# Kernel tuning notes

Hardware: AMD Instinct MI355X
Metric: run time of the kernel (lower is better)

## Reference

```python
import jax, jax.numpy as jnp
import numpy as np


def _ln(x):
    m = jnp.mean(x, axis=-1, keepdims=True)
    v = jnp.var(x, axis=-1, keepdims=True)
    return (x - m) * jax.lax.rsqrt(v + 1e-5)


def _forward(ql, cl, plm, ada_g_w, ada_g_b, ada_b_w, wq, bq, wk, wv, z_ln_g, z_ln_b, wz, wg, wo, sg_w, sg_b, ada2_g_w, ada2_g_b, ada2_b_w, ff1, ff2, ff3, sg2_w, sg2_b, n_queries, n_keys):
    B, N, C = ql.shape
    NB, _, D = wq.shape
    H = wz.shape[-1]
    DH = D // H
    # AF3-style 32x128 blocked local attention bias (additive mask), as in source
    centers = jnp.arange(N // n_queries + 1, dtype=jnp.float32) * n_queries + (n_queries / 2 - 0.5)
    pos = jnp.arange(N, dtype=jnp.float32)
    row = jnp.abs(pos[:, None] - centers[None, :]) < n_queries / 2   # [N, n_centers]
    col = jnp.abs(pos[:, None] - centers[None, :]) < n_keys / 2     # [N, n_centers]
    BIG = jnp.float32(1e10)
    blm = jnp.sum((row[:, None, :] & col[None, :, :]).astype(jnp.float32), axis=-1) * BIG - BIG  # [N, N], 0 or -1e10
    s_ln = _ln(cl)  # conditioning signal, shared LN across blocks
    a = ql
    for i in range(NB):  # DiffusionTransformer (AF3 Alg 23)
        # AttentionPairBias with AdaLN conditioning (Alg 24/26)
        x = jax.nn.sigmoid(s_ln @ ada_g_w[i] + ada_g_b[i]) * _ln(a) + s_ln @ ada_b_w[i]
        q = (x @ wq[i] + bq[i]).reshape(B, N, H, DH)
        k = (x @ wk[i]).reshape(B, N, H, DH)
        v = (x @ wv[i]).reshape(B, N, H, DH)
        zb = jnp.einsum('bqkc,ch->bhqk', _ln(plm) * z_ln_g[i] + z_ln_b[i], wz[i])  # pair bias
        logits = jnp.einsum('bqhd,bkhd->bhqk', q, k) * (1.0 / np.sqrt(DH)) + zb + blm[None, None]
        p = jax.nn.softmax(logits, axis=-1)
        o = jnp.einsum('bhqk,bkhd->bqhd', p, v)
        g = jax.nn.sigmoid(x @ wg[i]).reshape(B, N, H, DH)
        attn = (g * o).reshape(B, N, D) @ wo[i]
        b_out = jax.nn.sigmoid(s_ln @ sg_w[i] + sg_b[i]) * attn  # adaLN-zero style output gate
        # ConditionedTransitionBlock (Alg 25, SwiGLU)
        y = jax.nn.sigmoid(s_ln @ ada2_g_w[i] + ada2_g_b[i]) * _ln(a) + s_ln @ ada2_b_w[i]
        ff = jax.nn.silu(y @ ff1[i]) * (y @ ff2[i])
        t = jax.nn.sigmoid(s_ln @ sg2_w[i] + sg2_b[i]) * (ff @ ff3[i])
        a = b_out + t
    return a


def setup_inputs() -> dict:
    key = jax.random.key(0)
    B, N, C, CZ = 1, 3072, 128, 16
    H, DH, NB, CT = 4, 32, 3, 256  # CT = n_transition * C
    D = H * DH
    ks = jax.random.split(key, 32)
    it = iter(range(32))
    def r(shape, s=0.02):
        return jax.random.normal(ks[next(it)], shape, dtype=jnp.float32) * s
    inp = {
        'ql': jax.random.normal(ks[next(it)], (B, N, C), jnp.float32),
        'cl': jax.random.normal(ks[next(it)], (B, N, C), jnp.float32),
        'plm': jax.random.normal(ks[next(it)], (B, N, N, CZ), jnp.float32),
        'ada_g_w': r((NB, C, C)), 'ada_g_b': jnp.zeros((NB, C), jnp.float32), 'ada_b_w': r((NB, C, C)),
        'wq': r((NB, C, D)), 'bq': jnp.zeros((NB, D), jnp.float32), 'wk': r((NB, C, D)), 'wv': r((NB, C, D)),
        'z_ln_g': jnp.ones((NB, CZ), jnp.float32), 'z_ln_b': jnp.zeros((NB, CZ), jnp.float32), 'wz': r((NB, CZ, H)),
        'wg': r((NB, C, D)), 'wo': r((NB, D, C)),
        'sg_w': r((NB, C, C)), 'sg_b': jnp.full((NB, C), -2.0, jnp.float32),
        'ada2_g_w': r((NB, C, C)), 'ada2_g_b': jnp.zeros((NB, C), jnp.float32), 'ada2_b_w': r((NB, C, C)),
        'ff1': r((NB, C, CT)), 'ff2': r((NB, C, CT)), 'ff3': r((NB, CT, C)),
        'sg2_w': r((NB, C, C)), 'sg2_b': jnp.full((NB, C), -2.0, jnp.float32),
        'n_queries': 32, 'n_keys': 128,
    }
    return inp


def reference(ql, cl, plm, ada_g_w, ada_g_b, ada_b_w, wq, bq, wk, wv, z_ln_g, z_ln_b, wz, wg, wo, sg_w, sg_b, ada2_g_w, ada2_g_b, ada2_b_w, ff1, ff2, ff3, sg2_w, sg2_b, n_queries, n_keys):
    return _forward(ql, cl, plm, ada_g_w, ada_g_b, ada_b_w, wq, bq, wk, wv, z_ln_g, z_ln_b, wz, wg, wo, sg_w, sg_b, ada2_g_w, ada2_g_b, ada2_b_w, ff1, ff2, ff3, sg2_w, sg2_b, n_queries, n_keys)
```

## Files before the change

### kernel.cpp

```cpp
#include <hip/hip_runtime.h>
#include <cmath>

#define NTOK 3072
#define NBLK 3
#define PSS 133

__device__ __forceinline__ float sig(float v) { return 1.0f / (1.0f + expf(-v)); }

struct Params {
    const float *ql, *cl, *plm;
    const float *ada_g_w, *ada_g_b, *ada_b_w;
    const float *wq, *bq, *wk, *wv;
    const float *z_ln_g, *z_ln_b, *wz;
    const float *wg, *wo, *sg_w, *sg_b;
    const float *ada2_g_w, *ada2_g_b, *ada2_b_w;
    const float *ff1, *ff2, *ff3, *sg2_w, *sg2_b;
    float *qkvg, *ffb, *zb, *G, *bout4, *tpart;
    float *out;
};

__device__ __forceinline__ float4 ln_row32(float4 v)
{
    float s = v.x + v.y + v.z + v.w;
#pragma unroll
    for (int m = 1; m < 32; m <<= 1) s += __shfl_xor(s, m);
    float mean = s * (1.0f / 128.0f);
    float d0 = v.x - mean, d1 = v.y - mean, d2 = v.z - mean, d3 = v.w - mean;
    float var = d0 * d0 + d1 * d1 + d2 * d2 + d3 * d3;
#pragma unroll
    for (int m = 1; m < 32; m <<= 1) var += __shfl_xor(var, m);
    float rs = 1.0f / sqrtf(var * (1.0f / 128.0f) + 1e-5f);
    return make_float4(d0 * rs, d1 * rs, d2 * rs, d3 * rs);
}

__global__ __launch_bounds__(256) void k0_cond(Params P)
{
    int tid = threadIdx.x, bid = blockIdx.x;
    const size_t NC = (size_t)NTOK * 128;
    if (bid < 1728) {
        __shared__ __align__(16) float smA[32 * 132];
        int x8 = bid & 7, rest = bid >> 3;
        int tl = rest % 12, unit = rest / 12;
        int kind = unit % 6, i = unit / 6;
        int row0 = (x8 * 12 + tl) * 32;
#pragma unroll
        for (int it = 0; it < 4; it++) {
            int fo = (tid + it * 256) * 4, r = fo >> 7, c = fo & 127;
            *(float4*)&smA[r * 132 + c] = *(const float4*)&P.cl[(size_t)(row0 + r) * 128 + c];
        }
        __syncthreads();
        int hw = tid >> 5, cq = (tid & 31) * 4;
#pragma unroll
        for (int rr = 0; rr < 4; rr++) {
            int r = hw * 4 + rr;
            float4 n = ln_row32(*(float4*)&smA[r * 132 + cq]);
            *(float4*)&smA[r * 132 + cq] = n;
        }
        __syncthreads();
        const float* W; const float* bias = nullptr; bool dosig = false;
        switch (kind) {
            case 0:  W = P.ada_g_w  + (size_t)i * 16384; bias = P.ada_g_b  + i * 128; dosig = true; break;
            case 1:  W = P.ada_b_w  + (size_t)i * 16384; break;
            case 2:  W = P.ada2_g_w + (size_t)i * 16384; bias = P.ada2_g_b + i * 128; dosig = true; break;
            case 3:  W = P.ada2_b_w + (size_t)i * 16384; break;
            case 4:  W = P.sg_w     + (size_t)i * 16384; bias = P.sg_b     + i * 128; dosig = true; break;
            default: W = P.sg2_w    + (size_t)i * 16384; bias = P.sg2_b    + i * 128; dosig = true; break;
        }
        W += cq;
        float acc[4][4] = {};
#pragma unroll 8
        for (int k = 0; k < 128; k++) {
            float4 w4 = *(const float4*)(W + (size_t)k * 128);
#pragma unroll
            for (int rr = 0; rr < 4; rr++) {
                float a = smA[(hw * 4 + rr) * 132 + k];
                acc[rr][0] = fmaf(a, w4.x, acc[rr][0]);
                acc[rr][1] = fmaf(a, w4.y, acc[rr][1]);
                acc[rr][2] = fmaf(a, w4.z, acc[rr][2]);
                acc[rr][3] = fmaf(a, w4.w, acc[rr][3]);
            }
        }
        float4 b4 = bias ? *(const float4*)&bias[cq] : make_float4(0, 0, 0, 0);
        float* dst = P.G + (size_t)(kind * NBLK + i) * NC;
#pragma unroll
        for (int rr = 0; rr < 4; rr++) {
            float4 o = make_float4(acc[rr][0] + b4.x, acc[rr][1] + b4.y,
                                   acc[rr][2] + b4.z, acc[rr][3] + b4.w);
            if (dosig) { o.x = sig(o.x); o.y = sig(o.y); o.z = sig(o.z); o.w = sig(o.w); }
            *(float4*)&dst[(size_t)(row0 + hw * 4 + rr) * 128 + cq] = o;
        }
    } else {
        __shared__ __align__(16) float wzg[204];
        int b2 = bid - 1728;
        int x8 = b2 & 7, rest = b2 >> 3;
        int jl = rest >> 2, kkc = rest & 3;
        int j = x8 * 12 + jl;
        if (tid < 192) {
            int i3 = tid >> 6, rem = tid & 63, c = rem >> 2, h = rem & 3;
            wzg[(i3 * 16 + c) * 4 + h] = P.z_ln_g[i3 * 16 + c] * P.wz[(i3 * 16 + c) * 4 + h];
        }
        if (tid < 12) {
            int i3 = tid >> 2, h = tid & 3;
            float s = 0.0f;
            for (int c = 0; c < 16; c++) s += P.z_ln_b[i3 * 16 + c] * P.wz[(i3 * 16 + c) * 4 + h];
            wzg[192 + tid] = s;
        }
        __syncthreads();
        int kstart = max(0, j * 32 - 48);
        int W = min(NTOK, j * 32 + 80) - kstart;
#pragma unroll
        for (int it = 0; it < 4; it++) {
            int idx = tid + it * 256;
            int qi = idx >> 5, kk = kkc * 32 + (idx & 31);
            if (kk >= W) continue;
            int q = j * 32 + qi;
            const float* src = P.plm + ((size_t)q * NTOK + (size_t)(kstart + kk)) * 16;
            float xv[16];
            *(float4*)(xv + 0)  = *(const float4*)(src + 0);
            *(float4*)(xv + 4)  = *(const float4*)(src + 4);
            *(float4*)(xv + 8)  = *(const float4*)(src + 8);
            *(float4*)(xv + 12) = *(const float4*)(src + 12);
            float s = 0.0f;
#pragma unroll
            for (int c = 0; c < 16; c++) s += xv[c];
            float mean = s * (1.0f / 16.0f);
            float var = 0.0f;
#pragma unroll
            for (int c = 0; c < 16; c++) { float d = xv[c] - mean; var += d * d; }
            float rs = 1.0f / sqrtf(var * (1.0f / 16.0f) + 1e-5f);
#pragma unroll
            for (int c = 0; c < 16; c++) xv[c] = (xv[c] - mean) * rs;
#pragma unroll
            for (int i3 = 0; i3 < NBLK; i3++) {
#pragma unroll
                for (int h = 0; h < 4; h++) {
                    float o = wzg[192 + i3 * 4 + h];
#pragma unroll
                    for (int c = 0; c < 16; c++) o = fmaf(xv[c], wzg[(i3 * 16 + c) * 4 + h], o);
                    P.zb[((size_t)(i3 * 4 + h) * NTOK + q) * 128 + kk] = o;
                }
            }
        }
    }
}

__global__ __launch_bounds__(256) void kA_pre(Params P, int i)
{
    __shared__ __align__(16) float smX[32 * 132];
    const size_t NC = (size_t)NTOK * 128;
    int tid = threadIdx.x, bid = blockIdx.x;
    int x8 = bid & 7, rest = bid >> 3;
    int tl = rest % 12, u = rest / 12;
    int row0 = (x8 * 12 + tl) * 32;
    int hw = tid >> 5, cq = (tid & 31) * 4;
    const float* Gg = P.G + (size_t)(((u < 4 ? 0 : 2) * NBLK) + i) * NC;
    const float* Gb = P.G + (size_t)(((u < 4 ? 1 : 3) * NBLK) + i) * NC;
    const float* G4p = P.G + (size_t)(4 * NBLK + (i - 1)) * NC;
#pragma unroll
    for (int rr = 0; rr < 4; rr++) {
        int r = row0 + hw * 4 + rr;
        float4 a4;
        if (i == 0) {
            a4 = *(const float4*)&P.ql[(size_t)r * 128 + cq];
        } else {
            size_t off = (size_t)r * 128 + cq;
            float4 p0 = *(const float4*)&P.bout4[off];
            float4 p1 = *(const float4*)&P.bout4[NC + off];
            float4 p2 = *(const float4*)&P.bout4[2 * NC + off];
            float4 p3 = *(const float4*)&P.bout4[3 * NC + off];
            float4 tp = *(const float4*)&P.tpart[off];
            float4 gs = *(const float4*)&G4p[off];
            a4.x = fmaf(gs.x, p0.x + p1.x + p2.x + p3.x, tp.x);
            a4.y = fmaf(gs.y, p0.y + p1.y + p2.y + p3.y, tp.y);
            a4.z = fmaf(gs.z, p0.z + p1.z + p2.z + p3.z, tp.z);
            a4.w = fmaf(gs.w, p0.w + p1.w + p2.w + p3.w, tp.w);
        }
        float4 ln4 = ln_row32(a4);
        float4 g4 = *(const float4*)&Gg[(size_t)r * 128 + cq];
        float4 b4 = *(const float4*)&Gb[(size_t)r * 128 + cq];
        float4 x4;
        x4.x = fmaf(g4.x, ln4.x, b4.x);
        x4.y = fmaf(g4.y, ln4.y, b4.y);
        x4.z = fmaf(g4.z, ln4.z, b4.z);
        x4.w = fmaf(g4.w, ln4.w, b4.w);
        *(float4*)&smX[(hw * 4 + rr) * 132 + cq] = x4;
    }
    __syncthreads();
    if (u < 4) {
        const float* W = (u == 0 ? P.wq : u == 1 ? P.wk : u == 2 ? P.wv : P.wg)
                         + (size_t)i * 16384 + cq;
        float acc[4][4] = {};
#pragma unroll 8
        for (int k = 0; k < 128; k++) {
            float4 w4 = *(const float4*)(W + (size_t)k * 128);
#pragma unroll
            for (int rr = 0; rr < 4; rr++) {
                float a = smX[(hw * 4 + rr) * 132 + k];
                acc[rr][0] = fmaf(a, w4.x, acc[rr][0]);
                acc[rr][1] = fmaf(a, w4.y, acc[rr][1]);
                acc[rr][2] = fmaf(a, w4.z, acc[rr][2]);
                acc[rr][3] = fmaf(a, w4.w, acc[rr][3]);
            }
        }
        float4 b4 = (u == 0) ? *(const float4*)&P.bq[(size_t)i * 128 + cq]
                             : make_float4(0, 0, 0, 0);
#pragma unroll
        for (int rr = 0; rr < 4; rr++) {
            int r = row0 + hw * 4 + rr;
            *(float4*)&P.qkvg[(size_t)r * 512 + u * 128 + cq] =
                make_float4(acc[rr][0] + b4.x, acc[rr][1] + b4.y,
                            acc[rr][2] + b4.z, acc[rr][3] + b4.w);
        }
    } else {
        int ch = (u - 4) * 128;
        const float* W1 = P.ff1 + (size_t)i * 32768 + ch + cq;
        const float* W2 = P.ff2 + (size_t)i * 32768 + ch + cq;
        float a1[4][4] = {}, a2[4][4] = {};
#pragma unroll 4
        for (int k = 0; k < 128; k++) {
            float4 w14 = *(const float4*)(W1 + (size_t)k * 256);
            float4 w24 = *(const float4*)(W2 + (size_t)k * 256);
#pragma unroll
            for (int rr = 0; rr < 4; rr++) {
                float a = smX[(hw * 4 + rr) * 132 + k];
                a1[rr][0] = fmaf(a, w14.x, a1[rr][0]);
                a1[rr][1] = fmaf(a, w14.y, a1[rr][1]);
                a1[rr][2] = fmaf(a, w14.z, a1[rr][2]);
                a1[rr][3] = fmaf(a, w14.w, a1[rr][3]);
                a2[rr][0] = fmaf(a, w24.x, a2[rr][0]);
                a2[rr][1] = fmaf(a, w24.y, a2[rr][1]);
                a2[rr][2] = fmaf(a, w24.z, a2[rr][2]);
                a2[rr][3] = fmaf(a, w24.w, a2[rr][3]);
            }
        }
#pragma unroll
        for (int rr = 0; rr < 4; rr++) {
            int r = row0 + hw * 4 + rr;
            float4 o;
            o.x = a1[rr][0] * sig(a1[rr][0]) * a2[rr][0];
            o.y = a1[rr][1] * sig(a1[rr][1]) * a2[rr][1];
            o.z = a1[rr][2] * sig(a1[rr][2]) * a2[rr][2];
            o.w = a1[rr][3] * sig(a1[rr][3]) * a2[rr][3];
            *(float4*)&P.ffb[(size_t)r * 256 + ch + cq] = o;
        }
    }
}

__global__ __launch_bounds__(256) void kB_attn(Params P, int i)
{
    __shared__ __align__(16) float sm[11344];
    const size_t NC = (size_t)NTOK * 128;
    int tid = threadIdx.x, bid = blockIdx.x;
    if (bid < 768) {
        float* ks = sm;
        float* vs = sm + 4608;
        float* ps = sm + 9216;
        int x8 = bid & 7, g = bid >> 3;
        int jl = g >> 3, rem = g & 7;
        int h = rem >> 1, qh = rem & 1;
        int jglob = x8 * 12 + jl;
        int q0 = jglob * 32 + qh * 16;
        int kstart = max(0, jglob * 32 - 48);
        int W = min(NTOK, jglob * 32 + 80) - kstart;
        for (int idx = tid; idx < W * 8; idx += 256) {
            int kk = idx >> 3, d = (idx & 7) * 4;
            const float* base = &P.qkvg[(size_t)(kstart + kk) * 512 + 128 + h * 32 + d];
            float4 tK = *(const float4*)base;
            float4 tV = *(const float4*)(base + 128);
            *(float4*)&ks[kk * 36 + d] = tK;
            *(float4*)&vs[kk * 36 + d] = tV;
        }
        const float* zbase = &P.zb[((size_t)(i * 4 + h) * NTOK + q0) * 128];
#pragma unroll
        for (int it = 0; it < 2; it++) {
            int idx = tid + it * 256;
            int r = idx >> 5, c4 = (idx & 31) * 4;
            float4 z4 = *(const float4*)&zbase[(size_t)r * 128 + c4];
            ps[r * PSS + c4]     = z4.x;
            ps[r * PSS + c4 + 1] = z4.y;
            ps[r * PSS + c4 + 2] = z4.z;
            ps[r * PSS + c4 + 3] = z4.w;
        }
        int qi = tid & 15, kg = tid >> 4;
        float qreg[32];
        {
            const float* qp = &P.qkvg[(size_t)(q0 + qi) * 512 + h * 32];
#pragma unroll
            for (int d4 = 0; d4 < 8; d4++) {
                float4 tq = *(const float4*)(qp + d4 * 4);
                qreg[d4 * 4] = tq.x; qreg[d4 * 4 + 1] = tq.y;
                qreg[d4 * 4 + 2] = tq.z; qreg[d4 * 4 + 3] = tq.w;
            }
        }
        __syncthreads();
        const float scale = 0.17677669529663687f;
#pragma unroll
        for (int t2 = 0; t2 < 8; t2++) {
            int kk = kg + t2 * 16;
            if (kk < W) {
                float acc = 0.0f;
#pragma unroll
                for (int d4 = 0; d4 < 8; d4++) {
                    float4 kv = *(const float4*)&ks[kk * 36 + d4 * 4];
                    acc = fmaf(qreg[d4 * 4 + 0], kv.x, acc);
                    acc = fmaf(qreg[d4 * 4 + 1], kv.y, acc);
                    acc = fmaf(qreg[d4 * 4 + 2], kv.z, acc);
                    acc = fmaf(qreg[d4 * 4 + 3], kv.w, acc);
                }
                ps[qi * PSS + kk] = fmaf(acc, scale, ps[qi * PSS + kk]);
            }
        }
        __syncthreads();
        {
            int row = tid >> 4, sub = tid & 15;
            float m = -3.0e38f;
            for (int kk = sub; kk < W; kk += 16) m = fmaxf(m, ps[row * PSS + kk]);
#pragma unroll
            for (int s2 = 1; s2 < 16; s2 <<= 1) m = fmaxf(m, __shfl_xor(m, s2));
            float ssum = 0.0f;
            for (int kk = sub; kk < W; kk += 16) {
                float e = expf(ps[row * PSS + kk] - m);
                ps[row * PSS + kk] = e; ssum += e;
            }
#pragma unroll
            for (int s2 = 1; s2 < 16; s2 <<= 1) ssum += __shfl_xor(ssum, s2);
            float rinv = 1.0f / ssum;
            for (int kk = sub; kk < W; kk += 16) ps[row * PSS + kk] *= rinv;
        }
        __syncthreads();
        {
            int dg = tid >> 4, d0 = dg * 2;
            float o0 = 0.0f, o1 = 0.0f, o0b = 0.0f, o1b = 0.0f;
            for (int kk = 0; kk + 1 < W; kk += 2) {
                float p0 = ps[qi * PSS + kk], p1 = ps[qi * PSS + kk + 1];
                float2 va = *(const float2*)&vs[kk * 36 + d0];
                float2 vb = *(const float2*)&vs[(kk + 1) * 36 + d0];
                o0  = fmaf(p0, va.x, o0);  o1  = fmaf(p0, va.y, o1);
                o0b = fmaf(p1, vb.x, o0b); o1b = fmaf(p1, vb.y, o1b);
            }
            if (W & 1) {
                float p0 = ps[qi * PSS + W - 1];
                float2 va = *(const float2*)&vs[(W - 1) * 36 + d0];
                o0 = fmaf(p0, va.x, o0); o1 = fmaf(p0, va.y, o1);
            }
            o0 += o0b; o1 += o1b;
            float2 g2 = *(const float2*)&P.qkvg[(size_t)(q0 + qi) * 512 + 384 + h * 32 + d0];
            ks[qi * 33 + d0]     = o0 * sig(g2.x);
            ks[qi * 33 + d0 + 1] = o1 * sig(g2.y);
        }
        __syncthreads();
        {
            int r = tid >> 4, ci = tid & 15;
            int c0 = ci * 8;
            const float* o_s = ks;
            const float* wop = P.wo + (size_t)i * 16384 + (size_t)(h * 32) * 128 + c0;
            float acc[8] = {};
#pragma unroll 4
            for (int d = 0; d < 32; d++) {
                float a = o_s[r * 33 + d];
                float4 w0 = *(const float4*)(wop + (size_t)d * 128);
                float4 w1 = *(const float4*)(wop + (size_t)d * 128 + 4);
                acc[0] = fmaf(a, w0.x, acc[0]); acc[1] = fmaf(a, w0.y, acc[1]);
                acc[2] = fmaf(a, w0.z, acc[2]); acc[3] = fmaf(a, w0.w, acc[3]);
                acc[4] = fmaf(a, w1.x, acc[4]); acc[5] = fmaf(a, w1.y, acc[5]);
                acc[6] = fmaf(a, w1.z, acc[6]); acc[7] = fmaf(a, w1.w, acc[7]);
            }
            float* dst = P.bout4 + (size_t)h * NC + (size_t)(q0 + r) * 128 + c0;
            *(float4*)dst       = make_float4(acc[0], acc[1], acc[2], acc[3]);
            *(float4*)(dst + 4) = make_float4(acc[4], acc[5], acc[6], acc[7]);
        }
    } else {
        float* smC = sm;
        int b2 = bid - 768;
        int x8 = b2 & 7, rest = b2 >> 3;
        int tl = rest >> 1, chalf = rest & 1;
        int row0 = x8 * 384 + tl * 16;
#pragma unroll
        for (int it = 0; it < 4; it++) {
            int fo = (tid + it * 256) * 4, r = fo >> 8, c = fo & 255;
            *(float4*)&smC[r * 260 + c] = *(const float4*)&P.ffb[(size_t)(row0 + r) * 256 + c];
        }
        __syncthreads();
        int r = tid >> 4, c = chalf * 64 + (tid & 15) * 4;
        const float* f3_p = P.ff3 + (size_t)i * 32768 + c;
        float acc[4] = {};
#pragma unroll 8
        for (int k = 0; k < 256; k++) {
            float4 w4 = *(const float4*)(f3_p + (size_t)k * 128);
            float a = smC[r * 260 + k];
            acc[0] = fmaf(a, w4.x, acc[0]);
            acc[1] = fmaf(a, w4.y, acc[1]);
            acc[2] = fmaf(a, w4.z, acc[2]);
            acc[3] = fmaf(a, w4.w, acc[3]);
        }
        int row = row0 + r;
        float4 g5 = *(const float4*)&P.G[(size_t)(5 * NBLK + i) * NC + (size_t)row * 128 + c];
        *(float4*)&P.tpart[(size_t)row * 128 + c] =
            make_float4(g5.x * acc[0], g5.y * acc[1], g5.z * acc[2], g5.w * acc[3]);
    }
}

__global__ __launch_bounds__(256) void kC_out(Params P)
{
    const size_t NC = (size_t)NTOK * 128;
    int idx = blockIdx.x * 256 + threadIdx.x;
    int r = idx >> 5, cq = (idx & 31) * 4;
    size_t off = (size_t)r * 128 + cq;
    float4 p0 = *(const float4*)&P.bout4[off];
    float4 p1 = *(const float4*)&P.bout4[NC + off];
    float4 p2 = *(const float4*)&P.bout4[2 * NC + off];
    float4 p3 = *(const float4*)&P.bout4[3 * NC + off];
    float4 tp = *(const float4*)&P.tpart[off];
    float4 gs = *(const float4*)&P.G[(size_t)(4 * NBLK + (NBLK - 1)) * NC + off];
    float4 o;
    o.x = fmaf(gs.x, p0.x + p1.x + p2.x + p3.x, tp.x);
    o.y = fmaf(gs.y, p0.y + p1.y + p2.y + p3.y, tp.y);
    o.z = fmaf(gs.z, p0.z + p1.z + p2.z + p3.z, tp.z);
    o.w = fmaf(gs.w, p0.w + p1.w + p2.w + p3.w, tp.w);
    *(float4*)&P.out[off] = o;
}

extern "C" void kernel_launch(void* const* d_in, const int* in_sizes, int n_in,
                              void* d_out, int out_size, void* d_ws, size_t ws_size,
                              hipStream_t stream)
{
    Params P;
    P.ql       = (const float*)d_in[0];
    P.cl       = (const float*)d_in[1];
    P.plm      = (const float*)d_in[2];
    P.ada_g_w  = (const float*)d_in[3];
    P.ada_g_b  = (const float*)d_in[4];
    P.ada_b_w  = (const float*)d_in[5];
    P.wq       = (const float*)d_in[6];
    P.bq       = (const float*)d_in[7];
    P.wk       = (const float*)d_in[8];
    P.wv       = (const float*)d_in[9];
    P.z_ln_g   = (const float*)d_in[10];
    P.z_ln_b   = (const float*)d_in[11];
    P.wz       = (const float*)d_in[12];
    P.wg       = (const float*)d_in[13];
    P.wo       = (const float*)d_in[14];
    P.sg_w     = (const float*)d_in[15];
    P.sg_b     = (const float*)d_in[16];
    P.ada2_g_w = (const float*)d_in[17];
    P.ada2_g_b = (const float*)d_in[18];
    P.ada2_b_w = (const float*)d_in[19];
    P.ff1      = (const float*)d_in[20];
    P.ff2      = (const float*)d_in[21];
    P.ff3      = (const float*)d_in[22];
    P.sg2_w    = (const float*)d_in[23];
    P.sg2_b    = (const float*)d_in[24];

    float* ws = (float*)d_ws;
    const size_t NC = (size_t)NTOK * 128;
    P.qkvg  = ws;
    P.ffb   = ws + 4 * NC;
    P.zb    = ws + 6 * NC;
    P.G     = ws + 18 * NC;
    P.bout4 = ws + 36 * NC;
    P.tpart = ws + 40 * NC;
    P.out   = (float*)d_out;

    k0_cond<<<2112, 256, 0, stream>>>(P);
    for (int i = 0; i < NBLK; i++) {
        kA_pre<<<576, 256, 0, stream>>>(P, i);
        kB_attn<<<1152, 256, 0, stream>>>(P, i);
    }
    kC_out<<<384, 256, 0, stream>>>(P);
}
```

Baseline: 264.1 us.

## Accumulate block outputs with atomics and fold pair-bias into first pre kernel

Attention-head partials and the transition output are now gated and atomically added straight into a zeroed residual buffer, replacing the per-head bout4 and tpart buffers. The next block's pre kernel reads that buffer directly, and the final combine kernel is removed. The pair-bias computation moves from the conditioning kernel into the first pre-kernel launch so it runs alongside the QKV/FF projections. This cuts intermediate traffic and one launch, but adds scalar float atomics whose contention and nondeterministic summation order are the trade-off.

```diff
diff --git a/kernel.cpp b/kernel.cpp
--- a/kernel.cpp
+++ b/kernel.cpp
@@ -15,7 +15,8 @@
     const float *wg, *wo, *sg_w, *sg_b;
     const float *ada2_g_w, *ada2_g_b, *ada2_b_w;
     const float *ff1, *ff2, *ff3, *sg2_w, *sg2_b;
-    float *qkvg, *ffb, *zb, *G, *bout4, *tpart;
+    float *qkvg, *ffb, *zb, *G;
+    float *anew0, *anew1;
     float *out;
 };
 
@@ -35,63 +36,159 @@
 
 __global__ __launch_bounds__(256) void k0_cond(Params P)
 {
+    __shared__ __align__(16) float smA[32 * 132];
     int tid = threadIdx.x, bid = blockIdx.x;
     const size_t NC = (size_t)NTOK * 128;
-    if (bid < 1728) {
-        __shared__ __align__(16) float smA[32 * 132];
+    int x8 = bid & 7, rest = bid >> 3;
+    int tl = rest % 12, unit = rest / 12;
+    int kind = unit % 6, i = unit / 6;
+    int row0 = (x8 * 12 + tl) * 32;
+#pragma unroll
+    for (int it = 0; it < 4; it++) {
+        int fo = (tid + it * 256) * 4, r = fo >> 7, c = fo & 127;
+        *(float4*)&smA[r * 132 + c] = *(const float4*)&P.cl[(size_t)(row0 + r) * 128 + c];
+    }
+    __syncthreads();
+    int hw = tid >> 5, cq = (tid & 31) * 4;
+#pragma unroll
+    for (int rr = 0; rr < 4; rr++) {
+        int r = hw * 4 + rr;
+        float4 n = ln_row32(*(float4*)&smA[r * 132 + cq]);
+        *(float4*)&smA[r * 132 + cq] = n;
+    }
+    __syncthreads();
+    const float* W; const float* bias = nullptr; bool dosig = false;
+    switch (kind) {
+        case 0:  W = P.ada_g_w  + (size_t)i * 16384; bias = P.ada_g_b  + i * 128; dosig = true; break;
+        case 1:  W = P.ada_b_w  + (size_t)i * 16384; break;
+        case 2:  W = P.ada2_g_w + (size_t)i * 16384; bias = P.ada2_g_b + i * 128; dosig = true; break;
+        case 3:  W = P.ada2_b_w + (size_t)i * 16384; break;
+        case 4:  W = P.sg_w     + (size_t)i * 16384; bias = P.sg_b     + i * 128; dosig = true; break;
+        default: W = P.sg2_w    + (size_t)i * 16384; bias = P.sg2_b    + i * 128; dosig = true; break;
+    }
+    W += cq;
+    float acc[4][4] = {};
+#pragma unroll 8
+    for (int k = 0; k < 128; k++) {
+        float4 w4 = *(const float4*)(W + (size_t)k * 128);
+#pragma unroll
+        for (int rr = 0; rr < 4; rr++) {
+            float a = smA[(hw * 4 + rr) * 132 + k];
+            acc[rr][0] = fmaf(a, w4.x, acc[rr][0]);
+            acc[rr][1] = fmaf(a, w4.y, acc[rr][1]);
+            acc[rr][2] = fmaf(a, w4.z, acc[rr][2]);
+            acc[rr][3] = fmaf(a, w4.w, acc[rr][3]);
+        }
+    }
+    float4 b4 = bias ? *(const float4*)&bias[cq] : make_float4(0, 0, 0, 0);
+    float* dst = P.G + (size_t)(kind * NBLK + i) * NC;
+#pragma unroll
+    for (int rr = 0; rr < 4; rr++) {
+        float4 o = make_float4(acc[rr][0] + b4.x, acc[rr][1] + b4.y,
+                               acc[rr][2] + b4.z, acc[rr][3] + b4.w);
+        if (dosig) { o.x = sig(o.x); o.y = sig(o.y); o.z = sig(o.z); o.w = sig(o.w); }
+        *(float4*)&dst[(size_t)(row0 + hw * 4 + rr) * 128 + cq] = o;
+    }
+}
+
+__global__ __launch_bounds__(256) void kA_pre(Params P, int i,
+                                              const float* __restrict__ aprev,
+                                              float* __restrict__ dest)
+{
+    __shared__ __align__(16) float smX[32 * 132];
+    __shared__ __align__(16) float wzg[204];
+    const size_t NC = (size_t)NTOK * 128;
+    int tid = threadIdx.x, bid = blockIdx.x;
+    if (bid < 576) {
         int x8 = bid & 7, rest = bid >> 3;
-        int tl = rest % 12, unit = rest / 12;
-        int kind = unit % 6, i = unit / 6;
+        int tl = rest % 12, u = rest / 12;
         int row0 = (x8 * 12 + tl) * 32;
-#pragma unroll
-        for (int it = 0; it < 4; it++) {
-            int fo = (tid + it * 256) * 4, r = fo >> 7, c = fo & 127;
-            *(float4*)&smA[r * 132 + c] = *(const float4*)&P.cl[(size_t)(row0 + r) * 128 + c];
-        }
-        __syncthreads();
         int hw = tid >> 5, cq = (tid & 31) * 4;
+        if (u == 0) {
+            float4 z4 = make_float4(0, 0, 0, 0);
+#pragma unroll
+            for (int it = 0; it < 4; it++) {
+                int fo = (tid + it * 256) * 4, r = fo >> 7, c = fo & 127;
+                *(float4*)&dest[(size_t)(row0 + r) * 128 + c] = z4;
+            }
+        }
+        const float* Gg = P.G + (size_t)(((u < 4 ? 0 : 2) * NBLK) + i) * NC;
+        const float* Gb = P.G + (size_t)(((u < 4 ? 1 : 3) * NBLK) + i) * NC;
 #pragma unroll
         for (int rr = 0; rr < 4; rr++) {
-            int r = hw * 4 + rr;
-            float4 n = ln_row32(*(float4*)&smA[r * 132 + cq]);
-            *(float4*)&smA[r * 132 + cq] = n;
-        }
-        __syncthreads();
-        const float* W; const float* bias = nullptr; bool dosig = false;
-        switch (kind) {
-            case 0:  W = P.ada_g_w  + (size_t)i * 16384; bias = P.ada_g_b  + i * 128; dosig = true; break;
-            case 1:  W = P.ada_b_w  + (size_t)i * 16384; break;
-            case 2:  W = P.ada2_g_w + (size_t)i * 16384; bias = P.ada2_g_b + i * 128; dosig = true; break;
-            case 3:  W = P.ada2_b_w + (size_t)i * 16384; break;
-            case 4:  W = P.sg_w     + (size_t)i * 16384; bias = P.sg_b     + i * 128; dosig = true; break;
-            default: W = P.sg2_w    + (size_t)i * 16384; bias = P.sg2_b    + i * 128; dosig = true; break;
-        }
-        W += cq;
-        float acc[4][4] = {};
+            int r = row0 + hw * 4 + rr;
+            float4 a4 = *(const float4*)&aprev[(size_t)r * 128 + cq];
+            float4 ln4 = ln_row32(a4);
+            float4 g4 = *(const float4*)&Gg[(size_t)r * 128 + cq];
+            float4 b4 = *(const float4*)&Gb[(size_t)r * 128 + cq];
+            float4 x4;
+            x4.x = fmaf(g4.x, ln4.x, b4.x);
+            x4.y = fmaf(g4.y, ln4.y, b4.y);
+            x4.z = fmaf(g4.z, ln4.z, b4.z);
+            x4.w = fmaf(g4.w, ln4.w, b4.w);
+            *(float4*)&smX[(hw * 4 + rr) * 132 + cq] = x4;
+        }
+        __syncthreads();
+        if (u < 4) {
+            const float* W = (u == 0 ? P.wq : u == 1 ? P.wk : u == 2 ? P.wv : P.wg)
+                             + (size_t)i * 16384 + cq;
+            float acc[4][4] = {};
 #pragma unroll 8
-        for (int k = 0; k < 128; k++) {
-            float4 w4 = *(const float4*)(W + (size_t)k * 128);
+            for (int k = 0; k < 128; k++) {
+                float4 w4 = *(const float4*)(W + (size_t)k * 128);
+#pragma unroll
+                for (int rr = 0; rr < 4; rr++) {
+                    float a = smX[(hw * 4 + rr) * 132 + k];
+                    acc[rr][0] = fmaf(a, w4.x, acc[rr][0]);
+                    acc[rr][1] = fmaf(a, w4.y, acc[rr][1]);
+                    acc[rr][2] = fmaf(a, w4.z, acc[rr][2]);
+                    acc[rr][3] = fmaf(a, w4.w, acc[rr][3]);
+                }
+            }
+            float4 b4 = (u == 0) ? *(const float4*)&P.bq[(size_t)i * 128 + cq]
+                                 : make_float4(0, 0, 0, 0);
 #pragma unroll
             for (int rr = 0; rr < 4; rr++) {
-                float a = smA[(hw * 4 + rr) * 132 + k];
-                acc[rr][0] = fmaf(a, w4.x, acc[rr][0]);
-                acc[rr][1] = fmaf(a, w4.y, acc[rr][1]);
-                acc[rr][2] = fmaf(a, w4.z, acc[rr][2]);
-                acc[rr][3] = fmaf(a, w4.w, acc[rr][3]);
-            }
-        }
-        float4 b4 = bias ? *(const float4*)&bias[cq] : make_float4(0, 0, 0, 0);
-        float* dst = P.G + (size_t)(kind * NBLK + i) * NC;
-#pragma unroll
-        for (int rr = 0; rr < 4; rr++) {
-            float4 o = make_float4(acc[rr][0] + b4.x, acc[rr][1] + b4.y,
-                                   acc[rr][2] + b4.z, acc[rr][3] + b4.w);
-            if (dosig) { o.x = sig(o.x); o.y = sig(o.y); o.z = sig(o.z); o.w = sig(o.w); }
-            *(float4*)&dst[(size_t)(row0 + hw * 4 + rr) * 128 + cq] = o;
+                int r = row0 + hw * 4 + rr;
+                *(float4*)&P.qkvg[(size_t)r * 512 + u * 128 + cq] =
+                    make_float4(acc[rr][0] + b4.x, acc[rr][1] + b4.y,
+                                acc[rr][2] + b4.z, acc[rr][3] + b4.w);
+            }
+        } else {
+            int ch = (u - 4) * 128;
+            const float* W1 = P.ff1 + (size_t)i * 32768 + ch + cq;
+            const float* W2 = P.ff2 + (size_t)i * 32768 + ch + cq;
+            float a1[4][4] = {}, a2[4][4] = {};
+#pragma unroll 4
+            for (int k = 0; k < 128; k++) {
+                float4 w14 = *(const float4*)(W1 + (size_t)k * 256);
+                float4 w24 = *(const float4*)(W2 + (size_t)k * 256);
+#pragma unroll
+                for (int rr = 0; rr < 4; rr++) {
+                    float a = smX[(hw * 4 + rr) * 132 + k];
+                    a1[rr][0] = fmaf(a, w14.x, a1[rr][0]);
+                    a1[rr][1] = fmaf(a, w14.y, a1[rr][1]);
+                    a1[rr][2] = fmaf(a, w14.z, a1[rr][2]);
+                    a1[rr][3] = fmaf(a, w14.w, a1[rr][3]);
+                    a2[rr][0] = fmaf(a, w24.x, a2[rr][0]);
+                    a2[rr][1] = fmaf(a, w24.y, a2[rr][1]);
+                    a2[rr][2] = fmaf(a, w24.z, a2[rr][2]);
+                    a2[rr][3] = fmaf(a, w24.w, a2[rr][3]);
+                }
+            }
+#pragma unroll
+            for (int rr = 0; rr < 4; rr++) {
+                int r = row0 + hw * 4 + rr;
+                float4 o;
+                o.x = a1[rr][0] * sig(a1[rr][0]) * a2[rr][0];
+                o.y = a1[rr][1] * sig(a1[rr][1]) * a2[rr][1];
+                o.z = a1[rr][2] * sig(a1[rr][2]) * a2[rr][2];
+                o.w = a1[rr][3] * sig(a1[rr][3]) * a2[rr][3];
+                *(float4*)&P.ffb[(size_t)r * 256 + ch + cq] = o;
+            }
         }
     } else {
-        __shared__ __align__(16) float wzg[204];
-        int b2 = bid - 1728;
+        int b2 = bid - 576;
         int x8 = b2 & 7, rest = b2 >> 3;
         int jl = rest >> 2, kkc = rest & 3;
         int j = x8 * 12 + jl;
@@ -144,109 +241,7 @@
     }
 }
 
-__global__ __launch_bounds__(256) void kA_pre(Params P, int i)
-{
-    __shared__ __align__(16) float smX[32 * 132];
-    const size_t NC = (size_t)NTOK * 128;
-    int tid = threadIdx.x, bid = blockIdx.x;
-    int x8 = bid & 7, rest = bid >> 3;
-    int tl = rest % 12, u = rest / 12;
-    int row0 = (x8 * 12 + tl) * 32;
-    int hw = tid >> 5, cq = (tid & 31) * 4;
-    const float* Gg = P.G + (size_t)(((u < 4 ? 0 : 2) * NBLK) + i) * NC;
-    const float* Gb = P.G + (size_t)(((u < 4 ? 1 : 3) * NBLK) + i) * NC;
-    const float* G4p = P.G + (size_t)(4 * NBLK + (i - 1)) * NC;
-#pragma unroll
-    for (int rr = 0; rr < 4; rr++) {
-        int r = row0 + hw * 4 + rr;
-        float4 a4;
-        if (i == 0) {
-            a4 = *(const float4*)&P.ql[(size_t)r * 128 + cq];
-        } else {
-            size_t off = (size_t)r * 128 + cq;
-            float4 p0 = *(const float4*)&P.bout4[off];
-            float4 p1 = *(const float4*)&P.bout4[NC + off];
-            float4 p2 = *(const float4*)&P.bout4[2 * NC + off];
-            float4 p3 = *(const float4*)&P.bout4[3 * NC + off];
-            float4 tp = *(const float4*)&P.tpart[off];
-            float4 gs = *(const float4*)&G4p[off];
-            a4.x = fmaf(gs.x, p0.x + p1.x + p2.x + p3.x, tp.x);
-            a4.y = fmaf(gs.y, p0.y + p1.y + p2.y + p3.y, tp.y);
-            a4.z = fmaf(gs.z, p0.z + p1.z + p2.z + p3.z, tp.z);
-            a4.w = fmaf(gs.w, p0.w + p1.w + p2.w + p3.w, tp.w);
-        }
-        float4 ln4 = ln_row32(a4);
-        float4 g4 = *(const float4*)&Gg[(size_t)r * 128 + cq];
-        float4 b4 = *(const float4*)&Gb[(size_t)r * 128 + cq];
-        float4 x4;
-        x4.x = fmaf(g4.x, ln4.x, b4.x);
-        x4.y = fmaf(g4.y, ln4.y, b4.y);
-        x4.z = fmaf(g4.z, ln4.z, b4.z);
-        x4.w = fmaf(g4.w, ln4.w, b4.w);
-        *(float4*)&smX[(hw * 4 + rr) * 132 + cq] = x4;
-    }
-    __syncthreads();
-    if (u < 4) {
-        const float* W = (u == 0 ? P.wq : u == 1 ? P.wk : u == 2 ? P.wv : P.wg)
-                         + (size_t)i * 16384 + cq;
-        float acc[4][4] = {};
-#pragma unroll 8
-        for (int k = 0; k < 128; k++) {
-            float4 w4 = *(const float4*)(W + (size_t)k * 128);
-#pragma unroll
-            for (int rr = 0; rr < 4; rr++) {
-                float a = smX[(hw * 4 + rr) * 132 + k];
-                acc[rr][0] = fmaf(a, w4.x, acc[rr][0]);
-                acc[rr][1] = fmaf(a, w4.y, acc[rr][1]);
-                acc[rr][2] = fmaf(a, w4.z, acc[rr][2]);
-                acc[rr][3] = fmaf(a, w4.w, acc[rr][3]);
-            }
-        }
-        float4 b4 = (u == 0) ? *(const float4*)&P.bq[(size_t)i * 128 + cq]
-                             : make_float4(0, 0, 0, 0);
-#pragma unroll
-        for (int rr = 0; rr < 4; rr++) {
-            int r = row0 + hw * 4 + rr;
-            *(float4*)&P.qkvg[(size_t)r * 512 + u * 128 + cq] =
-                make_float4(acc[rr][0] + b4.x, acc[rr][1] + b4.y,
-                            acc[rr][2] + b4.z, acc[rr][3] + b4.w);
-        }
-    } else {
-        int ch = (u - 4) * 128;
-        const float* W1 = P.ff1 + (size_t)i * 32768 + ch + cq;
-        const float* W2 = P.ff2 + (size_t)i * 32768 + ch + cq;
-        float a1[4][4] = {}, a2[4][4] = {};
-#pragma unroll 4
-        for (int k = 0; k < 128; k++) {
-            float4 w14 = *(const float4*)(W1 + (size_t)k * 256);
-            float4 w24 = *(const float4*)(W2 + (size_t)k * 256);
-#pragma unroll
-            for (int rr = 0; rr < 4; rr++) {
-                float a = smX[(hw * 4 + rr) * 132 + k];
-                a1[rr][0] = fmaf(a, w14.x, a1[rr][0]);
-                a1[rr][1] = fmaf(a, w14.y, a1[rr][1]);
-                a1[rr][2] = fmaf(a, w14.z, a1[rr][2]);
-                a1[rr][3] = fmaf(a, w14.w, a1[rr][3]);
-                a2[rr][0] = fmaf(a, w24.x, a2[rr][0]);
-                a2[rr][1] = fmaf(a, w24.y, a2[rr][1]);
-                a2[rr][2] = fmaf(a, w24.z, a2[rr][2]);
-                a2[rr][3] = fmaf(a, w24.w, a2[rr][3]);
-            }
-        }
-#pragma unroll
-        for (int rr = 0; rr < 4; rr++) {
-            int r = row0 + hw * 4 + rr;
-            float4 o;
-            o.x = a1[rr][0] * sig(a1[rr][0]) * a2[rr][0];
-            o.y = a1[rr][1] * sig(a1[rr][1]) * a2[rr][1];
-            o.z = a1[rr][2] * sig(a1[rr][2]) * a2[rr][2];
-            o.w = a1[rr][3] * sig(a1[rr][3]) * a2[rr][3];
-            *(float4*)&P.ffb[(size_t)r * 256 + ch + cq] = o;
-        }
-    }
-}
-
-__global__ __launch_bounds__(256) void kB_attn(Params P, int i)
+__global__ __launch_bounds__(256) void kB_attn(Params P, int i, float* __restrict__ dest)
 {
     __shared__ __align__(16) float sm[11344];
     const size_t NC = (size_t)NTOK * 128;
@@ -365,9 +360,19 @@
                 acc[4] = fmaf(a, w1.x, acc[4]); acc[5] = fmaf(a, w1.y, acc[5]);
                 acc[6] = fmaf(a, w1.z, acc[6]); acc[7] = fmaf(a, w1.w, acc[7]);
             }
-            float* dst = P.bout4 + (size_t)h * NC + (size_t)(q0 + r) * 128 + c0;
-            *(float4*)dst       = make_float4(acc[0], acc[1], acc[2], acc[3]);
-            *(float4*)(dst + 4) = make_float4(acc[4], acc[5], acc[6], acc[7]);
+            size_t off = (size_t)(q0 + r) * 128 + c0;
+            const float* gsrow = &P.G[(size_t)(4 * NBLK + i) * NC + off];
+            float4 gs0 = *(const float4*)gsrow;
+            float4 gs1 = *(const float4*)(gsrow + 4);
+            float* dst = dest + off;
+            atomicAdd(dst + 0, gs0.x * acc[0]);
+            atomicAdd(dst + 1, gs0.y * acc[1]);
+            atomicAdd(dst + 2, gs0.z * acc[2]);
+            atomicAdd(dst + 3, gs0.w * acc[3]);
+            atomicAdd(dst + 4, gs1.x * acc[4]);
+            atomicAdd(dst + 5, gs1.y * acc[5]);
+            atomicAdd(dst + 6, gs1.z * acc[6]);
+            atomicAdd(dst + 7, gs1.w * acc[7]);
         }
     } else {
         float* smC = sm;
@@ -394,30 +399,14 @@
             acc[3] = fmaf(a, w4.w, acc[3]);
         }
         int row = row0 + r;
-        float4 g5 = *(const float4*)&P.G[(size_t)(5 * NBLK + i) * NC + (size_t)row * 128 + c];
-        *(float4*)&P.tpart[(size_t)row * 128 + c] =
-            make_float4(g5.x * acc[0], g5.y * acc[1], g5.z * acc[2], g5.w * acc[3]);
-    }
-}
-
-__global__ __launch_bounds__(256) void kC_out(Params P)
-{
-    const size_t NC = (size_t)NTOK * 128;
-    int idx = blockIdx.x * 256 + threadIdx.x;
-    int r = idx >> 5, cq = (idx & 31) * 4;
-    size_t off = (size_t)r * 128 + cq;
-    float4 p0 = *(const float4*)&P.bout4[off];
-    float4 p1 = *(const float4*)&P.bout4[NC + off];
-    float4 p2 = *(const float4*)&P.bout4[2 * NC + off];
-    float4 p3 = *(const float4*)&P.bout4[3 * NC + off];
-    float4 tp = *(const float4*)&P.tpart[off];
-    float4 gs = *(const float4*)&P.G[(size_t)(4 * NBLK + (NBLK - 1)) * NC + off];
-    float4 o;
-    o.x = fmaf(gs.x, p0.x + p1.x + p2.x + p3.x, tp.x);
-    o.y = fmaf(gs.y, p0.y + p1.y + p2.y + p3.y, tp.y);
-    o.z = fmaf(gs.z, p0.z + p1.z + p2.z + p3.z, tp.z);
-    o.w = fmaf(gs.w, p0.w + p1.w + p2.w + p3.w, tp.w);
-    *(float4*)&P.out[off] = o;
+        size_t off = (size_t)row * 128 + c;
+        float4 g5 = *(const float4*)&P.G[(size_t)(5 * NBLK + i) * NC + off];
+        float* dst = dest + off;
+        atomicAdd(dst + 0, g5.x * acc[0]);
+        atomicAdd(dst + 1, g5.y * acc[1]);
+        atomicAdd(dst + 2, g5.z * acc[2]);
+        atomicAdd(dst + 3, g5.w * acc[3]);
+    }
 }
 
 extern "C" void kernel_launch(void* const* d_in, const int* in_sizes, int n_in,
@@ -457,14 +446,16 @@
     P.ffb   = ws + 4 * NC;
     P.zb    = ws + 6 * NC;
     P.G     = ws + 18 * NC;
-    P.bout4 = ws + 36 * NC;
-    P.tpart = ws + 40 * NC;
+    P.anew0 = ws + 36 * NC;
+    P.anew1 = ws + 37 * NC;
     P.out   = (float*)d_out;
 
-    k0_cond<<<2112, 256, 0, stream>>>(P);
+    const float* aprev[NBLK] = { P.ql, P.anew0, P.anew1 };
+    float*       dest [NBLK] = { P.anew0, P.anew1, P.out };
+
+    k0_cond<<<1728, 256, 0, stream>>>(P);
     for (int i = 0; i < NBLK; i++) {
-        kA_pre<<<576, 256, 0, stream>>>(P, i);
-        kB_attn<<<1152, 256, 0, stream>>>(P, i);
-    }
-    kC_out<<<384, 256, 0, stream>>>(P);
+        kA_pre<<<(i == 0 ? 960 : 576), 256, 0, stream>>>(P, i, aprev[i], dest[i]);
+        kB_attn<<<1152, 256, 0, stream>>>(P, i, dest[i]);
+    }
 }
```

Result: slower. 348.9 us (+32.1%).

## Fuse block-0 pre-attention projections into the conditioning kernel and drop kA_pre launch

Applied to the files above, without the earlier changes.

The block-0 AdaLN modulation and the Q/K/V/G and FF1/FF2 projections now run inside k0_cond. That work depends only on the inputs, not on earlier blocks. The conditioning kernel no longer materialises block-0 AdaLN gate/bias tensors, and recomputes them in registers instead. This removes one kernel launch and the round trip of block-0 G tensors through global memory, and block-0 projection blocks overlap with the pair-bias and conditioning blocks in the same grid. The cost is redundant cl LayerNorm work and heavier new blocks with more registers.

```diff
diff --git a/kernel.cpp b/kernel.cpp
--- a/kernel.cpp
+++ b/kernel.cpp
@@ -35,13 +35,16 @@
 
 __global__ __launch_bounds__(256) void k0_cond(Params P)
 {
+    __shared__ __align__(16) float smA[32 * 132];
+    __shared__ __align__(16) float wzg[204];
     int tid = threadIdx.x, bid = blockIdx.x;
     const size_t NC = (size_t)NTOK * 128;
-    if (bid < 1728) {
-        __shared__ __align__(16) float smA[32 * 132];
+    if (bid < 1344) {
         int x8 = bid & 7, rest = bid >> 3;
         int tl = rest % 12, unit = rest / 12;
-        int kind = unit % 6, i = unit / 6;
+        int kind, i;
+        if (unit < 8) { kind = unit >> 1; i = 1 + (unit & 1); }
+        else          { int v = unit - 8; kind = 4 + v / 3; i = v % 3; }
         int row0 = (x8 * 12 + tl) * 32;
 #pragma unroll
         for (int it = 0; it < 4; it++) {
@@ -89,9 +92,8 @@
             if (dosig) { o.x = sig(o.x); o.y = sig(o.y); o.z = sig(o.z); o.w = sig(o.w); }
             *(float4*)&dst[(size_t)(row0 + hw * 4 + rr) * 128 + cq] = o;
         }
-    } else {
-        __shared__ __align__(16) float wzg[204];
-        int b2 = bid - 1728;
+    } else if (bid < 1728) {
+        int b2 = bid - 1344;
         int x8 = b2 & 7, rest = b2 >> 3;
         int jl = rest >> 2, kkc = rest & 3;
         int j = x8 * 12 + jl;
@@ -141,6 +143,118 @@
                 }
             }
         }
+    } else {
+        int b2 = bid - 1728;
+        int x8 = b2 & 7, rest = b2 >> 3;
+        int tl = rest % 12, u = rest / 12;
+        int row0 = (x8 * 12 + tl) * 32;
+        int hw = tid >> 5, cq = (tid & 31) * 4;
+#pragma unroll
+        for (int it = 0; it < 4; it++) {
+            int fo = (tid + it * 256) * 4, r = fo >> 7, c = fo & 127;
+            *(float4*)&smA[r * 132 + c] = *(const float4*)&P.cl[(size_t)(row0 + r) * 128 + c];
+        }
+        __syncthreads();
+#pragma unroll
+        for (int rr = 0; rr < 4; rr++) {
+            int r = hw * 4 + rr;
+            float4 n = ln_row32(*(float4*)&smA[r * 132 + cq]);
+            *(float4*)&smA[r * 132 + cq] = n;
+        }
+        __syncthreads();
+        const float* Wg = (u < 4 ? P.ada_g_w : P.ada2_g_w) + cq;
+        const float* Wb = (u < 4 ? P.ada_b_w : P.ada2_b_w) + cq;
+        const float* bg = (u < 4 ? P.ada_g_b : P.ada2_g_b);
+        float ga[4][4] = {}, ba[4][4] = {};
+#pragma unroll 4
+        for (int k = 0; k < 128; k++) {
+            float4 wg4 = *(const float4*)(Wg + (size_t)k * 128);
+            float4 wb4 = *(const float4*)(Wb + (size_t)k * 128);
+#pragma unroll
+            for (int rr = 0; rr < 4; rr++) {
+                float a = smA[(hw * 4 + rr) * 132 + k];
+                ga[rr][0] = fmaf(a, wg4.x, ga[rr][0]);
+                ga[rr][1] = fmaf(a, wg4.y, ga[rr][1]);
+                ga[rr][2] = fmaf(a, wg4.z, ga[rr][2]);
+                ga[rr][3] = fmaf(a, wg4.w, ga[rr][3]);
+                ba[rr][0] = fmaf(a, wb4.x, ba[rr][0]);
+                ba[rr][1] = fmaf(a, wb4.y, ba[rr][1]);
+                ba[rr][2] = fmaf(a, wb4.z, ba[rr][2]);
+                ba[rr][3] = fmaf(a, wb4.w, ba[rr][3]);
+            }
+        }
+        __syncthreads();
+        {
+            float4 bg4 = *(const float4*)&bg[cq];
+#pragma unroll
+            for (int rr = 0; rr < 4; rr++) {
+                int r = row0 + hw * 4 + rr;
+                float4 ln4 = ln_row32(*(const float4*)&P.ql[(size_t)r * 128 + cq]);
+                float4 x4;
+                x4.x = fmaf(sig(ga[rr][0] + bg4.x), ln4.x, ba[rr][0]);
+                x4.y = fmaf(sig(ga[rr][1] + bg4.y), ln4.y, ba[rr][1]);
+                x4.z = fmaf(sig(ga[rr][2] + bg4.z), ln4.z, ba[rr][2]);
+                x4.w = fmaf(sig(ga[rr][3] + bg4.w), ln4.w, ba[rr][3]);
+                *(float4*)&smA[(hw * 4 + rr) * 132 + cq] = x4;
+            }
+        }
+        __syncthreads();
+        if (u < 4) {
+            const float* W = (u == 0 ? P.wq : u == 1 ? P.wk : u == 2 ? P.wv : P.wg) + cq;
+            float acc[4][4] = {};
+#pragma unroll 8
+            for (int k = 0; k < 128; k++) {
+                float4 w4 = *(const float4*)(W + (size_t)k * 128);
+#pragma unroll
+                for (int rr = 0; rr < 4; rr++) {
+                    float a = smA[(hw * 4 + rr) * 132 + k];
+                    acc[rr][0] = fmaf(a, w4.x, acc[rr][0]);
+                    acc[rr][1] = fmaf(a, w4.y, acc[rr][1]);
+                    acc[rr][2] = fmaf(a, w4.z, acc[rr][2]);
+                    acc[rr][3] = fmaf(a, w4.w, acc[rr][3]);
+                }
+            }
+            float4 b4 = (u == 0) ? *(const float4*)&P.bq[cq] : make_float4(0, 0, 0, 0);
+#pragma unroll
+            for (int rr = 0; rr < 4; rr++) {
+                int r = row0 + hw * 4 + rr;
+                *(float4*)&P.qkvg[(size_t)r * 512 + u * 128 + cq] =
+                    make_float4(acc[rr][0] + b4.x, acc[rr][1] + b4.y,
+                                acc[rr][2] + b4.z, acc[rr][3] + b4.w);
+            }
+        } else {
+            int ch = (u - 4) * 128;
+            const float* W1 = P.ff1 + ch + cq;
+            const float* W2 = P.ff2 + ch + cq;
+            float a1[4][4] = {}, a2[4][4] = {};
+#pragma unroll 4
+            for (int k = 0; k < 128; k++) {
+                float4 w14 = *(const float4*)(W1 + (size_t)k * 256);
+                float4 w24 = *(const float4*)(W2 + (size_t)k * 256);
+#pragma unroll
+                for (int rr = 0; rr < 4; rr++) {
+                    float a = smA[(hw * 4 + rr) * 132 + k];
+                    a1[rr][0] = fmaf(a, w14.x, a1[rr][0]);
+                    a1[rr][1] = fmaf(a, w14.y, a1[rr][1]);
+                    a1[rr][2] = fmaf(a, w14.z, a1[rr][2]);
+                    a1[rr][3] = fmaf(a, w14.w, a1[rr][3]);
+                    a2[rr][0] = fmaf(a, w24.x, a2[rr][0]);
+                    a2[rr][1] = fmaf(a, w24.y, a2[rr][1]);
+                    a2[rr][2] = fmaf(a, w24.z, a2[rr][2]);
+                    a2[rr][3] = fmaf(a, w24.w, a2[rr][3]);
+                }
+            }
+#pragma unroll
+            for (int rr = 0; rr < 4; rr++) {
+                int r = row0 + hw * 4 + rr;
+                float4 o;
+                o.x = a1[rr][0] * sig(a1[rr][0]) * a2[rr][0];
+                o.y = a1[rr][1] * sig(a1[rr][1]) * a2[rr][1];
+                o.z = a1[rr][2] * sig(a1[rr][2]) * a2[rr][2];
+                o.w = a1[rr][3] * sig(a1[rr][3]) * a2[rr][3];
+                *(float4*)&P.ffb[(size_t)r * 256 + ch + cq] = o;
+            }
+        }
     }
 }
 
@@ -159,25 +273,21 @@
 #pragma unroll
     for (int rr = 0; rr < 4; rr++) {
         int r = row0 + hw * 4 + rr;
+        size_t off = (size_t)r * 128 + cq;
+        float4 p0 = *(const float4*)&P.bout4[off];
+        float4 p1 = *(const float4*)&P.bout4[NC + off];
+        float4 p2 = *(const float4*)&P.bout4[2 * NC + off];
+        float4 p3 = *(const float4*)&P.bout4[3 * NC + off];
+        float4 tp = *(const float4*)&P.tpart[off];
+        float4 gs = *(const float4*)&G4p[off];
         float4 a4;
-        if (i == 0) {
-            a4 = *(const float4*)&P.ql[(size_t)r * 128 + cq];
-        } else {
-            size_t off = (size_t)r * 128 + cq;
-            float4 p0 = *(const float4*)&P.bout4[off];
-            float4 p1 = *(const float4*)&P.bout4[NC + off];
-            float4 p2 = *(const float4*)&P.bout4[2 * NC + off];
-            float4 p3 = *(const float4*)&P.bout4[3 * NC + off];
-            float4 tp = *(const float4*)&P.tpart[off];
-            float4 gs = *(const float4*)&G4p[off];
-            a4.x = fmaf(gs.x, p0.x + p1.x + p2.x + p3.x, tp.x);
-            a4.y = fmaf(gs.y, p0.y + p1.y + p2.y + p3.y, tp.y);
-            a4.z = fmaf(gs.z, p0.z + p1.z + p2.z + p3.z, tp.z);
-            a4.w = fmaf(gs.w, p0.w + p1.w + p2.w + p3.w, tp.w);
-        }
+        a4.x = fmaf(gs.x, p0.x + p1.x + p2.x + p3.x, tp.x);
+        a4.y = fmaf(gs.y, p0.y + p1.y + p2.y + p3.y, tp.y);
+        a4.z = fmaf(gs.z, p0.z + p1.z + p2.z + p3.z, tp.z);
+        a4.w = fmaf(gs.w, p0.w + p1.w + p2.w + p3.w, tp.w);
         float4 ln4 = ln_row32(a4);
-        float4 g4 = *(const float4*)&Gg[(size_t)r * 128 + cq];
-        float4 b4 = *(const float4*)&Gb[(size_t)r * 128 + cq];
+        float4 g4 = *(const float4*)&Gg[off];
+        float4 b4 = *(const float4*)&Gb[off];
         float4 x4;
         x4.x = fmaf(g4.x, ln4.x, b4.x);
         x4.y = fmaf(g4.y, ln4.y, b4.y);
@@ -461,8 +571,9 @@
     P.tpart = ws + 40 * NC;
     P.out   = (float*)d_out;
 
-    k0_cond<<<2112, 256, 0, stream>>>(P);
-    for (int i = 0; i < NBLK; i++) {
+    k0_cond<<<2304, 256, 0, stream>>>(P);
+    kB_attn<<<1152, 256, 0, stream>>>(P, 0);
+    for (int i = 1; i < NBLK; i++) {
         kA_pre<<<576, 256, 0, stream>>>(P, i);
         kB_attn<<<1152, 256, 0, stream>>>(P, i);
     }
```

Result: slower. 278.4 us (+5.4%).
